# Kernel tuning notes

Hardware: AMD Instinct MI355X
Metric: run time of the kernel (lower is better)

## Reference

```python
import jax, jax.numpy as jnp
import numpy as np

N, E, B = 20000, 320000, 64
IN_DIM, HID, HEADS, NGF = 128, 64, 4, 9
NEG_SLOPE = 0.2
SET2SET_STEPS = 3


def _gat_conv(x, src, dst, W, a_src, a_dst, b, n):
    # PyG GATConv (eval mode): h = xW split into heads, edge score =
    # LeakyReLU(a_src.h[src] + a_dst.h[dst]), softmax over edges per dst node,
    # weighted scatter-sum of h[src], heads concatenated, + bias.
    H, C = a_src.shape
    h = (x @ W).reshape(n, H, C)                       # [N,H,C]
    s = jnp.sum(h * a_src, axis=-1)                    # [N,H]
    d = jnp.sum(h * a_dst, axis=-1)                    # [N,H]
    e = jax.nn.leaky_relu(s[src] + d[dst], NEG_SLOPE)  # [E,H]
    emax = jax.ops.segment_max(e, dst, num_segments=n)
    ex = jnp.exp(e - emax[dst])
    denom = jax.ops.segment_sum(ex, dst, num_segments=n)
    alpha = ex / (denom[dst] + 1e-16)                  # [E,H]
    out = jax.ops.segment_sum(h[src] * alpha[..., None], dst, num_segments=n)
    return out.reshape(n, H * C) + b


def _set2set(x, batch, Wih, Whh, bih, bhh, n_graphs):
    # Set2Set pooling: LSTM(q_star) -> attention over nodes per graph -> readout.
    d = x.shape[1]
    h = jnp.zeros((n_graphs, d), x.dtype)
    c = jnp.zeros((n_graphs, d), x.dtype)
    q_star = jnp.zeros((n_graphs, 2 * d), x.dtype)
    for _ in range(SET2SET_STEPS):
        gates = q_star @ Wih.T + bih + h @ Whh.T + bhh   # [B,4d], torch gate order i,f,g,o
        i, f, g, o = jnp.split(gates, 4, axis=1)
        c = jax.nn.sigmoid(f) * c + jax.nn.sigmoid(i) * jnp.tanh(g)
        h = jax.nn.sigmoid(o) * jnp.tanh(c)
        q = h                                            # [B,d]
        e = jnp.sum(x * q[batch], axis=-1)               # [N]
        emax = jax.ops.segment_max(e, batch, num_segments=n_graphs)
        a = jnp.exp(e - emax[batch])
        a = a / (jax.ops.segment_sum(a, batch, num_segments=n_graphs)[batch] + 1e-16)
        r = jax.ops.segment_sum(a[:, None] * x, batch, num_segments=n_graphs)  # [B,d]
        q_star = jnp.concatenate([q, r], axis=1)
    return q_star


def setup_inputs() -> dict:
    key = jax.random.key(0)
    ks = jax.random.split(key, 20)
    sc = 0.1
    inp = {
        "x": jax.random.normal(ks[0], (N, IN_DIM), jnp.float32),
        "edge_index": jax.random.randint(ks[1], (2, E), 0, N, dtype=jnp.int32),
        "batch": jnp.sort(jax.random.randint(ks[2], (N,), 0, B, dtype=jnp.int32)),
        "graph_features": jax.random.normal(ks[3], (B, NGF), jnp.float32),
        "W1": sc * jax.random.normal(ks[4], (IN_DIM, HEADS * HID), jnp.float32),
        "a_src1": sc * jax.random.normal(ks[5], (HEADS, HID), jnp.float32),
        "a_dst1": sc * jax.random.normal(ks[6], (HEADS, HID), jnp.float32),
        "b1": jnp.zeros((HEADS * HID,), jnp.float32),
        "W2": sc * jax.random.normal(ks[7], (HEADS * HID, HEADS * HID), jnp.float32),
        "a_src2": sc * jax.random.normal(ks[8], (HEADS, HID), jnp.float32),
        "a_dst2": sc * jax.random.normal(ks[9], (HEADS, HID), jnp.float32),
        "b2": jnp.zeros((HEADS * HID,), jnp.float32),
        "W3": sc * jax.random.normal(ks[10], (HEADS * HID, 2 * HID), jnp.float32),
        "a_src3": sc * jax.random.normal(ks[11], (1, 2 * HID), jnp.float32),
        "a_dst3": sc * jax.random.normal(ks[12], (1, 2 * HID), jnp.float32),
        "b3": jnp.zeros((2 * HID,), jnp.float32),
        "Wih": sc * jax.random.normal(ks[13], (4 * 2 * HID, 4 * HID), jnp.float32),
        "Whh": sc * jax.random.normal(ks[14], (4 * 2 * HID, 2 * HID), jnp.float32),
        "bih": jnp.zeros((4 * 2 * HID,), jnp.float32),
        "bhh": jnp.zeros((4 * 2 * HID,), jnp.float32),
        "gW1": sc * jax.random.normal(ks[15], (NGF, HID), jnp.float32),
        "gb1": jnp.zeros((HID,), jnp.float32),
        "gW2": sc * jax.random.normal(ks[16], (HID, HID // 2), jnp.float32),
        "gb2": jnp.zeros((HID // 2,), jnp.float32),
        "mW1": sc * jax.random.normal(ks[17], (2 * (2 * HID) + HID // 2, 128), jnp.float32),
        "mb1": jnp.zeros((128,), jnp.float32),
        "mW2": sc * jax.random.normal(ks[18], (128, 4), jnp.float32),
        "mb2": jnp.zeros((4,), jnp.float32),
    }
    return inp


def reference(x, edge_index, batch, graph_features,
              W1, a_src1, a_dst1, b1,
              W2, a_src2, a_dst2, b2,
              W3, a_src3, a_dst3, b3,
              Wih, Whh, bih, bhh,
              gW1, gb1, gW2, gb2,
              mW1, mb1, mW2, mb2):
    n = x.shape[0]
    # PyG GATConv default add_self_loops=True
    loops = jnp.arange(n, dtype=edge_index.dtype)
    src = jnp.concatenate([edge_index[0], loops])
    dst = jnp.concatenate([edge_index[1], loops])
    h = jax.nn.elu(_gat_conv(x, src, dst, W1, a_src1, a_dst1, b1, n))
    h = jax.nn.elu(_gat_conv(h, src, dst, W2, a_src2, a_dst2, b2, n))
    h = jax.nn.elu(_gat_conv(h, src, dst, W3, a_src3, a_dst3, b3, n))
    pooled = _set2set(h, batch, Wih, Whh, bih, bhh, B)              # [B, 256]
    gf = jax.nn.relu(graph_features @ gW1 + gb1) @ gW2 + gb2        # [B, 32]
    z = jnp.concatenate([pooled, gf], axis=1)                       # [B, 288]
    scores = jax.nn.relu(z @ mW1 + mb1) @ mW2 + mb2                 # [B, 4]
    return scores
```

## Files before the change

### kernel.cpp

```cpp
#include <hip/hip_runtime.h>
#include <hip/hip_bf16.h>
#include <math.h>

#define NEG_SLOPE 0.2f

typedef __attribute__((ext_vector_type(8))) short bf16x8;
typedef __attribute__((ext_vector_type(4))) float f32x4;

__device__ __forceinline__ float sigmoidf(float x){ return 1.f/(1.f+expf(-x)); }
__device__ __forceinline__ float bf2f(unsigned us){ return __uint_as_float(us << 16); }
__device__ __forceinline__ unsigned short bf16of(float v){
  __hip_bfloat16 h = __float2bfloat16(v);
  return __builtin_bit_cast(unsigned short, h);
}

__global__ void init_kernel(int* counts, int* gstart, int* gend,
                            float* rsum, float* lsum, float* sdbuf,
                            int* pad1, int* pad2, int npadints,
                            const float* __restrict__ W1, unsigned short* __restrict__ WT1,
                            const float* __restrict__ W2, unsigned short* __restrict__ WT2,
                            const float* __restrict__ W3, unsigned short* __restrict__ WT3,
                            int n, int b){
  int i = blockIdx.x*blockDim.x + threadIdx.x;
  if (i < n) counts[i] = 0;
  if (i < b){ gstart[i] = 0; gend[i] = 0; }
  if (i < 3*b*128) rsum[i] = 0.f;
  if (i < 3*b) lsum[i] = 0.f;
  if (i < 18*n) sdbuf[i] = 0.f;
  if (i < npadints){ pad1[i] = 0; pad2[i] = 0; }
  if (i < 128*256){
    int k = i>>8, c = i&255;
    WT1[(size_t)c*128 + k] = bf16of(W1[i]);
  }
  if (i < 256*256){
    int k = i>>8, c = i&255;
    WT2[(size_t)c*256 + k] = bf16of(W2[i]);
  }
  if (i < 256*128){
    int k = i>>7, c = i&127;
    WT3[(size_t)c*256 + k] = bf16of(W3[i]);
  }
}

__global__ void build_kernel(const int* __restrict__ ei, const int* __restrict__ batch,
                             int* counts, int* gstart, int* gend, int E, int n){
  int i = blockIdx.x*blockDim.x + threadIdx.x;
  if (i < E) atomicAdd(&counts[ei[E+i]], 1);
  if (i < n){
    int b = batch[i];
    if (i == 0 || batch[i-1] != b) gstart[b] = i;
    if (i == n-1 || batch[i+1] != b) gend[b] = i+1;
  }
}

__global__ void scan_kernel(const int* __restrict__ counts, int* offs, int* cursor, int n){
  const int T = 1024;
  int tid = threadIdx.x;
  int chunk = (n + T - 1)/T;
  int base = tid*chunk;
  int local = 0;
  for (int i=0;i<chunk;i++){ int idx=base+i; if (idx<n) local += counts[idx]; }
  __shared__ int ss[T];
  ss[tid]=local; __syncthreads();
  for (int off=1; off<T; off<<=1){
    int v = (tid>=off)? ss[tid-off] : 0;
    __syncthreads();
    ss[tid]+=v;
    __syncthreads();
  }
  int run = ss[tid]-local;
  for (int i=0;i<chunk;i++){
    int idx=base+i;
    if (idx<n){ offs[idx]=run; cursor[idx]=run; run += counts[idx]; }
  }
  if (tid==T-1) offs[n]=run;
}

__global__ void fill_kernel(const int* __restrict__ ei, int* cursor, int* csr, int E){
  int i = blockIdx.x*blockDim.x + threadIdx.x;
  if (i<E){
    int dst = ei[E+i];
    int pos = atomicAdd(&cursor[dst],1);
    csr[pos] = ei[i];
  }
}

template<bool AF32, int H>
__global__ __launch_bounds__(256) void gemm_bf16(
    const void* __restrict__ Aptr, const short* __restrict__ BT,
    unsigned short* __restrict__ Cb16,
    const float* __restrict__ asrc, const float* __restrict__ adst,
    float* __restrict__ sv, float* __restrict__ dv,
    int M, int Ktot, int N){
  __shared__ short As[64][72];
  __shared__ short Bs[128][72];
  int tid = threadIdx.x;
  int wave = tid>>6, lane = tid&63;
  int quad = lane>>4, l16 = lane&15;
  int bm = blockIdx.y*64, bn = blockIdx.x*128;
  f32x4 acc[8];
  #pragma unroll
  for (int i=0;i<8;i++) acc[i] = (f32x4){0.f,0.f,0.f,0.f};
  int rr = tid>>3;
  int seg = (tid&7)*8;
  int4 ra[2], rb[4];
  auto loadAB = [&](int k0){
    if (AF32){
      const float* A = (const float*)Aptr;
      #pragma unroll
      for (int p=0;p<2;p++){
        int row = bm + p*32 + rr;
        float4 v0 = make_float4(0.f,0.f,0.f,0.f), v1 = v0;
        if (row < M){
          const float* ap = A + (size_t)row*Ktot + k0 + seg;
          v0 = *(const float4*)(ap);
          v1 = *(const float4*)(ap+4);
        }
        unsigned u0 = (unsigned)bf16of(v0.x) | ((unsigned)bf16of(v0.y)<<16);
        unsigned u1 = (unsigned)bf16of(v0.z) | ((unsigned)bf16of(v0.w)<<16);
        unsigned u2 = (unsigned)bf16of(v1.x) | ((unsigned)bf16of(v1.y)<<16);
        unsigned u3 = (unsigned)bf16of(v1.z) | ((unsigned)bf16of(v1.w)<<16);
        ra[p] = make_int4((int)u0,(int)u1,(int)u2,(int)u3);
      }
    } else {
      const short* A = (const short*)Aptr;
      #pragma unroll
      for (int p=0;p<2;p++)
        ra[p] = *(const int4*)(A + (size_t)(bm + p*32 + rr)*Ktot + k0 + seg);
    }
    #pragma unroll
    for (int p=0;p<4;p++)
      rb[p] = *(const int4*)(BT + (size_t)(bn + p*32 + rr)*Ktot + k0 + seg);
  };
  loadAB(0);
  for (int k0=0; k0<Ktot; k0+=64){
    __syncthreads();
    #pragma unroll
    for (int p=0;p<2;p++) *(int4*)&As[p*32+rr][seg] = ra[p];
    #pragma unroll
    for (int p=0;p<4;p++) *(int4*)&Bs[p*32+rr][seg] = rb[p];
    __syncthreads();
    if (k0+64 < Ktot) loadAB(k0+64);
    #pragma unroll
    for (int kk=0;kk<2;kk++){
      bf16x8 af = *(bf16x8*)&As[wave*16 + l16][kk*32 + quad*8];
      #pragma unroll
      for (int nf=0;nf<8;nf++){
        bf16x8 bfv = *(bf16x8*)&Bs[nf*16 + l16][kk*32 + quad*8];
        acc[nf] = __builtin_amdgcn_mfma_f32_16x16x32_bf16(af, bfv, acc[nf], 0,0,0);
      }
    }
  }
  float av[8], bv[8];
  #pragma unroll
  for (int nf=0;nf<8;nf++){
    int c = bn + nf*16 + l16;
    av[nf] = asrc[c];
    bv[nf] = adst[c];
  }
  #pragma unroll
  for (int r=0;r<4;r++){
    int row = bm + wave*16 + quad*4 + r;
    float psA=0.f, pdA=0.f, psB=0.f, pdB=0.f;
    #pragma unroll
    for (int nf=0;nf<4;nf++){ psA += acc[nf][r]*av[nf]; pdA += acc[nf][r]*bv[nf]; }
    #pragma unroll
    for (int nf=4;nf<8;nf++){ psB += acc[nf][r]*av[nf]; pdB += acc[nf][r]*bv[nf]; }
    #pragma unroll
    for (int off=1; off<16; off<<=1){
      psA += __shfl_xor(psA,off); pdA += __shfl_xor(pdA,off);
      psB += __shfl_xor(psB,off); pdB += __shfl_xor(pdB,off);
    }
    if (l16==0 && row < M){
      if (H == 4){
        int h0 = bn>>6;
        atomicAdd(&sv[row*4 + h0],     psA);
        atomicAdd(&dv[row*4 + h0],     pdA);
        atomicAdd(&sv[row*4 + h0 + 1], psB);
        atomicAdd(&dv[row*4 + h0 + 1], pdB);
      } else {
        atomicAdd(&sv[row], psA + psB);
        atomicAdd(&dv[row], pdA + pdB);
      }
    }
  }
  __syncthreads();
  unsigned short* stgS = (unsigned short*)(&As[0][0]) + wave*1056;
  #pragma unroll
  for (int r=0;r<4;r++){
    #pragma unroll
    for (int nf=0;nf<8;nf++)
      stgS[quad*264 + nf*16 + l16] = bf16of(acc[nf][r]);
    int row = bm + wave*16 + quad*4 + r;
    if (row < M){
      int4 v = *(int4*)(stgS + quad*264 + l16*8);
      *(int4*)(Cb16 + (size_t)row*N + bn + l16*8) = v;
    }
  }
}

template<int H, int C, bool SPLIT>
__global__ __launch_bounds__(256) void agg_kernel(
    const unsigned short* __restrict__ hb, const float* __restrict__ s,
    const float* __restrict__ d, const int* __restrict__ offs,
    const int* __restrict__ csr, const float* __restrict__ bias,
    float* __restrict__ yf, unsigned short* __restrict__ ys, int n_nodes){
  constexpr int HC = H*C;
  constexpr int SLICES = HC/64;
  int bx = blockIdx.x;
  int sl = bx % SLICES;
  int ng = bx / SLICES;
  int tid = threadIdx.x;
  int grp = tid >> 4;
  int l4  = tid & 15;
  int n = ng*16 + grp;
  if (n >= n_nodes) return;
  int c0 = sl*64 + l4*4;
  int head = c0 / C;
  float ddst = d[n*H + head];
  int start = offs[n];
  int cnt = offs[n+1] - start;
  int cnt1 = cnt + 1;
  float a0=0.f, a1=0.f, a2=0.f, a3=0.f, lp=0.f;
  for (int base=0; base<cnt1; base+=16){
    int nchunk = min(16, cnt1-base);
    int srcv = 0; float wv = 0.f;
    if (l4 < nchunk){
      int i = base + l4;
      srcv = (i==cnt) ? n : csr[start+i];
      float e = s[srcv*H + head] + ddst;
      e = e>=0.f ? e : NEG_SLOPE*e;
      wv = expf(e);
      lp += wv;
    }
    for (int j=0;j<nchunk;j++){
      int sj = __shfl(srcv, j, 16);
      float wj = __shfl(wv, j, 16);
      int2 hv = *reinterpret_cast<const int2*>(hb + (size_t)sj*HC + c0);
      a0 += wj*bf2f((unsigned)hv.x & 0xFFFFu);
      a1 += wj*bf2f((unsigned)hv.x >> 16);
      a2 += wj*bf2f((unsigned)hv.y & 0xFFFFu);
      a3 += wj*bf2f((unsigned)hv.y >> 16);
    }
  }
  #pragma unroll
  for (int off=1; off<16; off<<=1) lp += __shfl_xor(lp, off, 16);
  float inv = 1.f/(lp + 1e-16f);
  float o[4] = {a0*inv, a1*inv, a2*inv, a3*inv};
  #pragma unroll
  for (int v=0;v<4;v++){
    float t = o[v] + bias[c0+v];
    o[v] = t>0.f ? t : expm1f(t);
  }
  if (SPLIT){
    unsigned u0 = (unsigned)bf16of(o[0]) | ((unsigned)bf16of(o[1])<<16);
    unsigned u1 = (unsigned)bf16of(o[2]) | ((unsigned)bf16of(o[3])<<16);
    *reinterpret_cast<uint2*>(ys + (size_t)n*HC + c0) = make_uint2(u0,u1);
  } else {
    float4 fv = make_float4(o[0], o[1], o[2], o[3]);
    *reinterpret_cast<float4*>(yf + (size_t)n*HC + c0) = fv;
  }
}

__global__ __launch_bounds__(256) void read_kernel(
    const float* __restrict__ x, const float* __restrict__ q,
    const int* __restrict__ batch,
    float* __restrict__ rsum, float* __restrict__ lsum, int N){
  int tid = threadIdx.x;
  int wave = tid>>6, lane = tid&63;
  int c0 = blockIdx.x*32;
  if (c0 >= N) return;
  __shared__ float ws[32];
  __shared__ int gb[32];
  if (tid < 32 && c0+tid < N) gb[tid] = batch[c0+tid];
  __syncthreads();
  #pragma unroll
  for (int j=0;j<8;j++){
    int k = wave*8 + j;
    int i = c0 + k;
    if (i < N){
      int g = gb[k];
      float2 xv = *reinterpret_cast<const float2*>(x + (size_t)i*128 + lane*2);
      float2 qv = *reinterpret_cast<const float2*>(q + (size_t)g*128 + lane*2);
      float p = xv.x*qv.x + xv.y*qv.y;
      #pragma unroll
      for (int off=32; off; off>>=1) p += __shfl_down(p, off);
      if (lane==0) ws[k] = expf(p);
    }
  }
  __syncthreads();
  if (tid < 128){
    int col = tid;
    int endi = min(c0+32, N);
    int curg = gb[0];
    float acc = 0.f, lacc = 0.f;
    for (int i=c0; i<endi; ++i){
      int g = gb[i-c0];
      if (g != curg){
        atomicAdd(&rsum[curg*128+col], acc);
        if (col==0) atomicAdd(&lsum[curg], lacc);
        acc = 0.f; lacc = 0.f; curg = g;
      }
      float w = ws[i-c0];
      acc += w * x[(size_t)i*128+col];
      lacc += w;
    }
    atomicAdd(&rsum[curg*128+col], acc);
    if (col==0) atomicAdd(&lsum[curg], lacc);
  }
}

template<int STEP>
__global__ __launch_bounds__(256) void s2s_step_kernel(
    const float* __restrict__ rsum, const float* __restrict__ lsum,
    float* __restrict__ hc, float* __restrict__ qbuf,
    const float* __restrict__ Wih, const float* __restrict__ Whh,
    const float* __restrict__ bih, const float* __restrict__ bhh,
    const float* __restrict__ gfeat,
    const float* __restrict__ gW1, const float* __restrict__ gb1,
    const float* __restrict__ gW2, const float* __restrict__ gb2,
    const float* __restrict__ mW1, const float* __restrict__ mb1,
    const float* __restrict__ mW2, const float* __restrict__ mb2,
    float* __restrict__ out, int B){
  int b = blockIdx.x, tid = threadIdx.x;
  __shared__ float qs[256];

  if (STEP > 0){
    if (tid < 128){
      const float* rs = rsum + (size_t)(STEP-1)*B*128 + (size_t)b*128;
      float ls = lsum[(STEP-1)*B + b];
      qs[tid]     = qbuf[b*128+tid];
      qs[128+tid] = rs[tid] / (ls + 1e-16f);
    }
    __syncthreads();
  }

  if (STEP < 3){
    __shared__ float hs[128], gsh[512];
    if (STEP > 0){ if (tid<128) hs[tid] = hc[(size_t)b*128+tid]; }
    __syncthreads();
    #pragma unroll
    for (int p=0;p<2;p++){
      int j = tid + p*256;
      float a = bih[j] + bhh[j];
      if (STEP > 0){
        const float* wi = Wih + (size_t)j*256;
        for (int k=0;k<256;k+=4)
          a += qs[k]*wi[k] + qs[k+1]*wi[k+1] + qs[k+2]*wi[k+2] + qs[k+3]*wi[k+3];
        const float* wh = Whh + (size_t)j*128;
        for (int k=0;k<128;k+=4)
          a += hs[k]*wh[k] + hs[k+1]*wh[k+1] + hs[k+2]*wh[k+2] + hs[k+3]*wh[k+3];
      }
      gsh[j] = a;
    }
    __syncthreads();
    if (tid < 128){
      float cprev = (STEP==0) ? 0.f : hc[(size_t)(B+b)*128+tid];
      float ig = sigmoidf(gsh[tid]);
      float fg = sigmoidf(gsh[128+tid]);
      float gg = tanhf(gsh[256+tid]);
      float og = sigmoidf(gsh[384+tid]);
      float c2 = fg*cprev + ig*gg;
      float h2 = og*tanhf(c2);
      hc[(size_t)b*128+tid] = h2;
      hc[(size_t)(B+b)*128+tid] = c2;
      qbuf[b*128+tid] = h2;
    }
  } else {
    __shared__ float z[288], gf1[64], hid[128];
    z[tid] = qs[tid];
    if (tid < 64){
      float a = gb1[tid];
      for (int k=0;k<9;k++) a += gfeat[b*9+k]*gW1[k*64+tid];
      gf1[tid] = a>0.f ? a : 0.f;
    }
    __syncthreads();
    if (tid < 32){
      float a = gb2[tid];
      for (int k=0;k<64;k++) a += gf1[k]*gW2[k*32+tid];
      z[256+tid] = a;
    }
    __syncthreads();
    if (tid < 128){
      float a = mb1[tid];
      for (int k=0;k<288;k++) a += z[k]*mW1[(size_t)k*128+tid];
      hid[tid] = a>0.f ? a : 0.f;
    }
    __syncthreads();
    if (tid < 4){
      float a = mb2[tid];
      for (int k=0;k<128;k++) a += hid[k]*mW2[k*4+tid];
      out[b*4+tid] = a;
    }
  }
}

extern "C" void kernel_launch(void* const* d_in, const int* in_sizes, int n_in,
                              void* d_out, int out_size, void* d_ws, size_t ws_size,
                              hipStream_t stream) {
  const float* x     = (const float*)d_in[0];
  const int*   ei    = (const int*)d_in[1];
  const int*   batch = (const int*)d_in[2];
  const float* gfeat = (const float*)d_in[3];
  const float* W1    = (const float*)d_in[4];
  const float* as1   = (const float*)d_in[5];
  const float* ad1   = (const float*)d_in[6];
  const float* b1    = (const float*)d_in[7];
  const float* W2    = (const float*)d_in[8];
  const float* as2   = (const float*)d_in[9];
  const float* ad2   = (const float*)d_in[10];
  const float* b2    = (const float*)d_in[11];
  const float* W3    = (const float*)d_in[12];
  const float* as3   = (const float*)d_in[13];
  const float* ad3   = (const float*)d_in[14];
  const float* b3    = (const float*)d_in[15];
  const float* Wih   = (const float*)d_in[16];
  const float* Whh   = (const float*)d_in[17];
  const float* bih   = (const float*)d_in[18];
  const float* bhh   = (const float*)d_in[19];
  const float* gW1   = (const float*)d_in[20];
  const float* gb1   = (const float*)d_in[21];
  const float* gW2   = (const float*)d_in[22];
  const float* gb2   = (const float*)d_in[23];
  const float* mW1   = (const float*)d_in[24];
  const float* mb1   = (const float*)d_in[25];
  const float* mW2   = (const float*)d_in[26];
  const float* mb2   = (const float*)d_in[27];

  const int N = in_sizes[0]/128;
  const int E = in_sizes[1]/2;
  const int B = in_sizes[3]/9;
  const int Mpad = ((N + 127)/128)*128;

  char* ws = (char*)d_ws;
  size_t off = 0;
  auto alloc = [&](size_t bytes)->char*{
    char* p = ws + off;
    off += (bytes + 255) & ~(size_t)255;
    return p;
  };
  unsigned short* hb16 = (unsigned short*)alloc((size_t)N*256*2);
  unsigned short* y1   = (unsigned short*)alloc((size_t)Mpad*256*2);
  unsigned short* y2   = (unsigned short*)alloc((size_t)Mpad*256*2);
  float*    ybuf    = (float*)alloc((size_t)N*128*4);
  unsigned short* WT1 = (unsigned short*)alloc((size_t)256*128*2);
  unsigned short* WT2 = (unsigned short*)alloc((size_t)256*256*2);
  unsigned short* WT3 = (unsigned short*)alloc((size_t)128*256*2);
  float* sdbuf  = (float*)alloc((size_t)18*N*4);
  int*   counts = (int*)alloc((size_t)N*4);
  int*   offs   = (int*)alloc((size_t)(N+1)*4);
  int*   cursor = (int*)alloc((size_t)N*4);
  int*   csr    = (int*)alloc((size_t)E*4);
  int*   gstart = (int*)alloc((size_t)B*4);
  int*   gend   = (int*)alloc((size_t)B*4);
  float* hcbuf  = (float*)alloc((size_t)2*B*128*4);
  float* qbuf   = (float*)alloc((size_t)B*128*4);
  float* rsum   = (float*)alloc((size_t)3*B*128*4);
  float* lsum   = (float*)alloc((size_t)3*B*4);

  float* s1 = sdbuf;            float* d1 = sdbuf + (size_t)4*N;
  float* s2 = sdbuf + (size_t)8*N;  float* d2 = sdbuf + (size_t)12*N;
  float* s3 = sdbuf + (size_t)16*N; float* d3 = sdbuf + (size_t)17*N;

  int npadints = (Mpad - N)*128;
  int nInit = 18*N;
  if (npadints > nInit) nInit = npadints;
  if (256*256 > nInit) nInit = 256*256;
  init_kernel<<<(nInit+255)/256, 256, 0, stream>>>(counts, gstart, gend,
      rsum, lsum, sdbuf,
      (int*)(y1 + (size_t)N*256), (int*)(y2 + (size_t)N*256),
      npadints, W1, WT1, W2, WT2, W3, WT3, N, B);
  int gridEN = (max(E,N)+255)/256;
  build_kernel<<<gridEN, 256, 0, stream>>>(ei, batch, counts, gstart, gend, E, N);
  scan_kernel<<<1, 1024, 0, stream>>>(counts, offs, cursor, N);
  fill_kernel<<<(E+255)/256, 256, 0, stream>>>(ei, cursor, csr, E);

  int gm = Mpad/64;
  int ng16 = (N+15)/16;
  gemm_bf16<true,4><<<dim3(2,gm), 256, 0, stream>>>((const void*)x, (const short*)WT1,
      hb16, as1, ad1, s1, d1, N, 128, 256);
  agg_kernel<4,64,true><<<ng16*4, 256, 0, stream>>>(hb16, s1, d1, offs, csr, b1, nullptr, y1, N);
  gemm_bf16<false,4><<<dim3(2,gm), 256, 0, stream>>>((const void*)y1, (const short*)WT2,
      hb16, as2, ad2, s2, d2, N, 256, 256);
  agg_kernel<4,64,true><<<ng16*4, 256, 0, stream>>>(hb16, s2, d2, offs, csr, b2, nullptr, y2, N);
  gemm_bf16<false,1><<<dim3(1,gm), 256, 0, stream>>>((const void*)y2, (const short*)WT3,
      hb16, as3, ad3, s3, d3, N, 256, 128);
  agg_kernel<1,128,false><<<ng16*2, 256, 0, stream>>>(hb16, s3, d3, offs, csr, b3, ybuf, nullptr, N);

  int gr = (N+31)/32;
  s2s_step_kernel<0><<<B, 256, 0, stream>>>(rsum, lsum, hcbuf, qbuf,
      Wih, Whh, bih, bhh, gfeat, gW1, gb1, gW2, gb2, mW1, mb1, mW2, mb2, (float*)d_out, B);
  read_kernel<<<gr, 256, 0, stream>>>(ybuf, qbuf, batch, rsum + 0*(size_t)B*128, lsum + 0*B, N);
  s2s_step_kernel<1><<<B, 256, 0, stream>>>(rsum, lsum, hcbuf, qbuf,
      Wih, Whh, bih, bhh, gfeat, gW1, gb1, gW2, gb2, mW1, mb1, mW2, mb2, (float*)d_out, B);
  read_kernel<<<gr, 256, 0, stream>>>(ybuf, qbuf, batch, rsum + 1*(size_t)B*128, lsum + 1*B, N);
  s2s_step_kernel<2><<<B, 256, 0, stream>>>(rsum, lsum, hcbuf, qbuf,
      Wih, Whh, bih, bhh, gfeat, gW1, gb1, gW2, gb2, mW1, mb1, mW2, mb2, (float*)d_out, B);
  read_kernel<<<gr, 256, 0, stream>>>(ybuf, qbuf, batch, rsum + 2*(size_t)B*128, lsum + 2*B, N);
  s2s_step_kernel<3><<<B, 256, 0, stream>>>(rsum, lsum, hcbuf, qbuf,
      Wih, Whh, bih, bhh, gfeat, gW1, gb1, gW2, gb2, mW1, mb1, mW2, mb2, (float*)d_out, B);
}
```

Baseline: 453.3 us.

## Fuse Set2Set steps and readouts into one per-graph kernel

Replaces the alternating LSTM-step and readout kernels (seven launches) with a single kernel where each block owns one graph's contiguous node range and runs all three Set2Set iterations plus the MLP head. LSTM state stays in shared memory and the readout uses block reductions instead of global atomics. This removes launch gaps and atomic traffic, but limits the pooling stage to one block per graph, so far fewer CUs do the memory streaming.

```diff
diff --git a/kernel.cpp b/kernel.cpp
--- a/kernel.cpp
+++ b/kernel.cpp
@@ -14,8 +14,7 @@
   return __builtin_bit_cast(unsigned short, h);
 }
 
-__global__ void init_kernel(int* counts, int* gstart, int* gend,
-                            float* rsum, float* lsum, float* sdbuf,
+__global__ void init_kernel(int* counts, int* gstart, int* gend, float* sdbuf,
                             int* pad1, int* pad2, int npadints,
                             const float* __restrict__ W1, unsigned short* __restrict__ WT1,
                             const float* __restrict__ W2, unsigned short* __restrict__ WT2,
@@ -24,8 +23,6 @@
   int i = blockIdx.x*blockDim.x + threadIdx.x;
   if (i < n) counts[i] = 0;
   if (i < b){ gstart[i] = 0; gend[i] = 0; }
-  if (i < 3*b*128) rsum[i] = 0.f;
-  if (i < 3*b) lsum[i] = 0.f;
   if (i < 18*n) sdbuf[i] = 0.f;
   if (i < npadints){ pad1[i] = 0; pad2[i] = 0; }
   if (i < 128*256){
@@ -262,58 +259,9 @@
   }
 }
 
-__global__ __launch_bounds__(256) void read_kernel(
-    const float* __restrict__ x, const float* __restrict__ q,
-    const int* __restrict__ batch,
-    float* __restrict__ rsum, float* __restrict__ lsum, int N){
-  int tid = threadIdx.x;
-  int wave = tid>>6, lane = tid&63;
-  int c0 = blockIdx.x*32;
-  if (c0 >= N) return;
-  __shared__ float ws[32];
-  __shared__ int gb[32];
-  if (tid < 32 && c0+tid < N) gb[tid] = batch[c0+tid];
-  __syncthreads();
-  #pragma unroll
-  for (int j=0;j<8;j++){
-    int k = wave*8 + j;
-    int i = c0 + k;
-    if (i < N){
-      int g = gb[k];
-      float2 xv = *reinterpret_cast<const float2*>(x + (size_t)i*128 + lane*2);
-      float2 qv = *reinterpret_cast<const float2*>(q + (size_t)g*128 + lane*2);
-      float p = xv.x*qv.x + xv.y*qv.y;
-      #pragma unroll
-      for (int off=32; off; off>>=1) p += __shfl_down(p, off);
-      if (lane==0) ws[k] = expf(p);
-    }
-  }
-  __syncthreads();
-  if (tid < 128){
-    int col = tid;
-    int endi = min(c0+32, N);
-    int curg = gb[0];
-    float acc = 0.f, lacc = 0.f;
-    for (int i=c0; i<endi; ++i){
-      int g = gb[i-c0];
-      if (g != curg){
-        atomicAdd(&rsum[curg*128+col], acc);
-        if (col==0) atomicAdd(&lsum[curg], lacc);
-        acc = 0.f; lacc = 0.f; curg = g;
-      }
-      float w = ws[i-c0];
-      acc += w * x[(size_t)i*128+col];
-      lacc += w;
-    }
-    atomicAdd(&rsum[curg*128+col], acc);
-    if (col==0) atomicAdd(&lsum[curg], lacc);
-  }
-}
-
-template<int STEP>
-__global__ __launch_bounds__(256) void s2s_step_kernel(
-    const float* __restrict__ rsum, const float* __restrict__ lsum,
-    float* __restrict__ hc, float* __restrict__ qbuf,
+__global__ __launch_bounds__(256) void s2s_all_kernel(
+    const float* __restrict__ x, const int* __restrict__ gstart,
+    const int* __restrict__ gend, float* __restrict__ e_ws,
     const float* __restrict__ Wih, const float* __restrict__ Whh,
     const float* __restrict__ bih, const float* __restrict__ bhh,
     const float* __restrict__ gfeat,
@@ -321,29 +269,20 @@
     const float* __restrict__ gW2, const float* __restrict__ gb2,
     const float* __restrict__ mW1, const float* __restrict__ mb1,
     const float* __restrict__ mW2, const float* __restrict__ mb2,
-    float* __restrict__ out, int B){
+    float* __restrict__ out){
   int b = blockIdx.x, tid = threadIdx.x;
-  __shared__ float qs[256];
-
-  if (STEP > 0){
-    if (tid < 128){
-      const float* rs = rsum + (size_t)(STEP-1)*B*128 + (size_t)b*128;
-      float ls = lsum[(STEP-1)*B + b];
-      qs[tid]     = qbuf[b*128+tid];
-      qs[128+tid] = rs[tid] / (ls + 1e-16f);
-    }
-    __syncthreads();
-  }
-
-  if (STEP < 3){
-    __shared__ float hs[128], gsh[512];
-    if (STEP > 0){ if (tid<128) hs[tid] = hc[(size_t)b*128+tid]; }
-    __syncthreads();
+  int wave = tid>>6, lane = tid&63;
+  __shared__ float qs[256], hs[128], cs[128], gsh[512], red[256], lsh[2];
+  int start = gstart[b], end = gend[b];
+  if (tid < 128){ hs[tid]=0.f; cs[tid]=0.f; }
+  qs[tid] = 0.f;
+  __syncthreads();
+  for (int step=0; step<3; ++step){
     #pragma unroll
     for (int p=0;p<2;p++){
       int j = tid + p*256;
       float a = bih[j] + bhh[j];
-      if (STEP > 0){
+      if (step > 0){
         const float* wi = Wih + (size_t)j*256;
         for (int k=0;k<256;k+=4)
           a += qs[k]*wi[k] + qs[k+1]*wi[k+1] + qs[k+2]*wi[k+2] + qs[k+3]*wi[k+3];
@@ -355,43 +294,68 @@
     }
     __syncthreads();
     if (tid < 128){
-      float cprev = (STEP==0) ? 0.f : hc[(size_t)(B+b)*128+tid];
       float ig = sigmoidf(gsh[tid]);
       float fg = sigmoidf(gsh[128+tid]);
       float gg = tanhf(gsh[256+tid]);
       float og = sigmoidf(gsh[384+tid]);
-      float c2 = fg*cprev + ig*gg;
-      float h2 = og*tanhf(c2);
-      hc[(size_t)b*128+tid] = h2;
-      hc[(size_t)(B+b)*128+tid] = c2;
-      qbuf[b*128+tid] = h2;
-    }
-  } else {
-    __shared__ float z[288], gf1[64], hid[128];
-    z[tid] = qs[tid];
-    if (tid < 64){
-      float a = gb1[tid];
-      for (int k=0;k<9;k++) a += gfeat[b*9+k]*gW1[k*64+tid];
-      gf1[tid] = a>0.f ? a : 0.f;
-    }
-    __syncthreads();
-    if (tid < 32){
-      float a = gb2[tid];
-      for (int k=0;k<64;k++) a += gf1[k]*gW2[k*32+tid];
-      z[256+tid] = a;
-    }
+      float c2 = fg*cs[tid] + ig*gg;
+      cs[tid] = c2;
+      hs[tid] = og*tanhf(c2);
+    }
+    __syncthreads();
+    float q0 = hs[lane*2], q1 = hs[lane*2+1];
+    for (int i = start + wave; i < end; i += 4){
+      float2 xv = *reinterpret_cast<const float2*>(x + (size_t)i*128 + lane*2);
+      float p = xv.x*q0 + xv.y*q1;
+      #pragma unroll
+      for (int off=32; off; off>>=1) p += __shfl_down(p, off);
+      if (lane==0) e_ws[i] = expf(p);
+    }
+    __syncthreads();
+    int half = tid >> 7, col = tid & 127;
+    float rc = 0.f, ls = 0.f;
+    #pragma unroll 4
+    for (int i=start+half; i<end; i+=2){
+      float w = e_ws[i];
+      rc += w * x[(size_t)i*128+col];
+      if (col==0) ls += w;
+    }
+    if (tid < 2) lsh[tid]=0.f;
+    __syncthreads();
+    red[tid] = rc;
+    if (col==0) lsh[half] = ls;
     __syncthreads();
     if (tid < 128){
-      float a = mb1[tid];
-      for (int k=0;k<288;k++) a += z[k]*mW1[(size_t)k*128+tid];
-      hid[tid] = a>0.f ? a : 0.f;
-    }
-    __syncthreads();
-    if (tid < 4){
-      float a = mb2[tid];
-      for (int k=0;k<128;k++) a += hid[k]*mW2[k*4+tid];
-      out[b*4+tid] = a;
-    }
+      float r = (red[tid]+red[tid+128])/(lsh[0]+lsh[1]+1e-16f);
+      qs[tid]     = hs[tid];
+      qs[128+tid] = r;
+    }
+    __syncthreads();
+  }
+  __shared__ float z[288], gf1[64], hid[128];
+  z[tid] = qs[tid];
+  if (tid < 64){
+    float a = gb1[tid];
+    for (int k=0;k<9;k++) a += gfeat[b*9+k]*gW1[k*64+tid];
+    gf1[tid] = a>0.f ? a : 0.f;
+  }
+  __syncthreads();
+  if (tid < 32){
+    float a = gb2[tid];
+    for (int k=0;k<64;k++) a += gf1[k]*gW2[k*32+tid];
+    z[256+tid] = a;
+  }
+  __syncthreads();
+  if (tid < 128){
+    float a = mb1[tid];
+    for (int k=0;k<288;k++) a += z[k]*mW1[(size_t)k*128+tid];
+    hid[tid] = a>0.f ? a : 0.f;
+  }
+  __syncthreads();
+  if (tid < 4){
+    float a = mb2[tid];
+    for (int k=0;k<128;k++) a += hid[k]*mW2[k*4+tid];
+    out[b*4+tid] = a;
   }
 }
 
@@ -447,16 +411,13 @@
   unsigned short* WT2 = (unsigned short*)alloc((size_t)256*256*2);
   unsigned short* WT3 = (unsigned short*)alloc((size_t)128*256*2);
   float* sdbuf  = (float*)alloc((size_t)18*N*4);
+  float* e_ws   = (float*)alloc((size_t)N*4);
   int*   counts = (int*)alloc((size_t)N*4);
   int*   offs   = (int*)alloc((size_t)(N+1)*4);
   int*   cursor = (int*)alloc((size_t)N*4);
   int*   csr    = (int*)alloc((size_t)E*4);
   int*   gstart = (int*)alloc((size_t)B*4);
   int*   gend   = (int*)alloc((size_t)B*4);
-  float* hcbuf  = (float*)alloc((size_t)2*B*128*4);
-  float* qbuf   = (float*)alloc((size_t)B*128*4);
-  float* rsum   = (float*)alloc((size_t)3*B*128*4);
-  float* lsum   = (float*)alloc((size_t)3*B*4);
 
   float* s1 = sdbuf;            float* d1 = sdbuf + (size_t)4*N;
   float* s2 = sdbuf + (size_t)8*N;  float* d2 = sdbuf + (size_t)12*N;
@@ -466,8 +427,7 @@
   int nInit = 18*N;
   if (npadints > nInit) nInit = npadints;
   if (256*256 > nInit) nInit = 256*256;
-  init_kernel<<<(nInit+255)/256, 256, 0, stream>>>(counts, gstart, gend,
-      rsum, lsum, sdbuf,
+  init_kernel<<<(nInit+255)/256, 256, 0, stream>>>(counts, gstart, gend, sdbuf,
       (int*)(y1 + (size_t)N*256), (int*)(y2 + (size_t)N*256),
       npadints, W1, WT1, W2, WT2, W3, WT3, N, B);
   int gridEN = (max(E,N)+255)/256;
@@ -487,16 +447,7 @@
       hb16, as3, ad3, s3, d3, N, 256, 128);
   agg_kernel<1,128,false><<<ng16*2, 256, 0, stream>>>(hb16, s3, d3, offs, csr, b3, ybuf, nullptr, N);
 
-  int gr = (N+31)/32;
-  s2s_step_kernel<0><<<B, 256, 0, stream>>>(rsum, lsum, hcbuf, qbuf,
-      Wih, Whh, bih, bhh, gfeat, gW1, gb1, gW2, gb2, mW1, mb1, mW2, mb2, (float*)d_out, B);
-  read_kernel<<<gr, 256, 0, stream>>>(ybuf, qbuf, batch, rsum + 0*(size_t)B*128, lsum + 0*B, N);
-  s2s_step_kernel<1><<<B, 256, 0, stream>>>(rsum, lsum, hcbuf, qbuf,
-      Wih, Whh, bih, bhh, gfeat, gW1, gb1, gW2, gb2, mW1, mb1, mW2, mb2, (float*)d_out, B);
-  read_kernel<<<gr, 256, 0, stream>>>(ybuf, qbuf, batch, rsum + 1*(size_t)B*128, lsum + 1*B, N);
-  s2s_step_kernel<2><<<B, 256, 0, stream>>>(rsum, lsum, hcbuf, qbuf,
-      Wih, Whh, bih, bhh, gfeat, gW1, gb1, gW2, gb2, mW1, mb1, mW2, mb2, (float*)d_out, B);
-  read_kernel<<<gr, 256, 0, stream>>>(ybuf, qbuf, batch, rsum + 2*(size_t)B*128, lsum + 2*B, N);
-  s2s_step_kernel<3><<<B, 256, 0, stream>>>(rsum, lsum, hcbuf, qbuf,
-      Wih, Whh, bih, bhh, gfeat, gW1, gb1, gW2, gb2, mW1, mb1, mW2, mb2, (float*)d_out, B);
-}
+  s2s_all_kernel<<<B, 256, 0, stream>>>(ybuf, gstart, gend, e_ws,
+      Wih, Whh, bih, bhh, gfeat, gW1, gb1, gW2, gb2, mW1, mb1, mW2, mb2,
+      (float*)d_out);
+}
```

New measurement: 526.8 us. 1.16x slower.
